# Kernel tuning notes

Measured on AMD Instinct MI355X. Metric: run time of the kernel, lower is better.

Reference implementation:

```python
import jax, jax.numpy as jnp
import numpy as np

B, C, W, H = 32, 128, 128, 128  # batch, channels, window_size, prediction_horizon
KAPPA = 10.0

def setup_inputs() -> dict:
    key = jax.random.key(0)
    k1, k2, k3, k4 = jax.random.split(key, 4)
    x_t = jax.random.normal(k1, (B, C, W), dtype=jnp.float32)
    # d are observation timestamps in [0, H), compared against ref_t = linspace(0, H, H)
    d = jax.random.uniform(k2, (B, C, W), dtype=jnp.float32) * H
    # m is an observation mask/weight in (0, 1]; avoid exact zeros for log(m)
    m = jax.random.uniform(k3, (B, C, W), dtype=jnp.float32, minval=1e-3, maxval=1.0)
    kernel = jax.random.normal(k4, (W,), dtype=jnp.float32) * 0.1
    return {"x_t": x_t, "d": d, "m": m, "kernel": kernel}

def reference(x_t, d, m, kernel):
    # ref_t: [H], matches torch.linspace(0, H, H)
    ref_t = jnp.linspace(0.0, H, H, dtype=x_t.dtype)
    # norm: [B,C,W,H] squared time differences
    norm = (d[..., None] - ref_t) ** 2
    alpha = jnp.log1p(jnp.exp(kernel))[None, None, :, None]  # softplus, [1,1,W,1]
    logm = jnp.log(m)[..., None]                             # [B,C,W,1]
    # low-intensity interpolation (softmax over window dim W)
    s = -alpha * norm + logm                                 # [B,C,W,H]
    w = jax.nn.logsumexp(s, axis=2)                          # [B,C,H]
    w1 = jnp.exp(s - w[:, :, None, :])                       # softmax weights
    y = jnp.einsum('bcwh,bcw->bch', w1, x_t)
    # high-intensity (transient) interpolation with sharper kernel kappa*alpha
    s_t = -KAPPA * alpha * norm + logm
    wt_lse = jax.nn.logsumexp(s_t, axis=2)
    w_t = jnp.exp(s_t - wt_lse[:, :, None, :])
    y_trans = jnp.einsum('bcwh,bcw->bch', w_t, x_t)
    return (y, w, y_trans)
```

## Files before the change

kernel.cpp:

```cpp
#include <hip/hip_runtime.h>
#include <hip/hip_bf16.h>

#define NB 32
#define NC 128
#define NW 128
#define NH 128
#define BCH (NB * NC * NH)

__global__ __launch_bounds__(128, 4) void sci_kernel(
    const void* __restrict__ xp, const void* __restrict__ dp,
    const void* __restrict__ mp, const void* __restrict__ kp,
    void* __restrict__ outp)
{
    const int bc   = blockIdx.x;
    const int tid  = threadIdx.x;
    const int lane = tid & 63;
    const int wid  = tid >> 6;

    __shared__ float4 tileS[NW];
    __shared__ float2 tileA[NW];
    __shared__ int    cum[NW + 1];
    __shared__ int    wtot[2];
    __shared__ float  wmin[2];

    const unsigned short* du16 = (const unsigned short*)dp;
    bool is_bf16 = true;
    #pragma unroll
    for (int i = 0; i < 32; i += 2) {
        float v = __uint_as_float(((unsigned int)du16[i]) << 16);
        is_bf16 = is_bf16 && (v >= 0.0f) && (v <= 129.0f);
    }

    float dv, mv, xv, kv;
    {
        const int base = bc * NW + tid;
        if (is_bf16) {
            dv = __bfloat162float(((const __hip_bfloat16*)dp)[base]);
            mv = __bfloat162float(((const __hip_bfloat16*)mp)[base]);
            xv = __bfloat162float(((const __hip_bfloat16*)xp)[base]);
            kv = __bfloat162float(((const __hip_bfloat16*)kp)[tid]);
        } else {
            dv = ((const float*)dp)[base];
            mv = ((const float*)mp)[base];
            xv = ((const float*)xp)[base];
            kv = ((const float*)kp)[tid];
        }
    }
    const float LOG2E = 1.4426950408889634f;
    float A2  = log1pf(__expf(kv)) * LOG2E;
    float sA2 = sqrtf(A2);
    float sd  = sA2 * dv;

    float rmn = sA2;
    #pragma unroll
    for (int o = 32; o >= 1; o >>= 1) rmn = fminf(rmn, __shfl_xor(rmn, o));
    if (lane == 0) wmin[wid] = rmn;

    cum[tid] = 0;
    __syncthreads();
    int bin  = min(127, max(0, (int)dv));
    int slot = atomicAdd(&cum[bin], 1);
    __syncthreads();

    int cnt = cum[tid];
    int c = cnt;
    #pragma unroll
    for (int o = 1; o < 64; o <<= 1) {
        int n = __shfl_up(c, o);
        if (lane >= o) c += n;
    }
    if (lane == 63) wtot[wid] = c;
    __syncthreads();
    int excl = c - cnt + (wid ? wtot[0] : 0);
    cum[tid] = excl;
    if (tid == 0) cum[NW] = NW;
    __syncthreads();

    int pos = cum[bin] + slot;
    tileS[pos] = make_float4(sA2, sd, mv, mv * xv);
    tileA[pos] = make_float2(sA2, sd);
    __syncthreads();

    const float rsA2min = (1.0f / fminf(wmin[0], wmin[1])) * 1.0005f;

    const float rh = (float)tid * (128.0f / 127.0f);

    int b0 = min(127, (int)rh);
    int s0, e0;
    {
        int r = 0;
        do {
            int lo = max(0, b0 - r);
            int hi = min(127, b0 + r);
            s0 = cum[lo]; e0 = cum[hi + 1];
            ++r;
        } while (s0 == e0);
    }
    float mn0 = 1e30f;
    for (int k = s0; k < e0; ++k) {
        float2 q = tileA[k];
        float t = __builtin_fmaf(-q.x, rh, q.y);
        mn0 = fminf(mn0, t * t);
    }

    float Rh = sqrtf(mn0 + 30.0f) * rsA2min;
    int lo = max(0, (int)(rh - Rh));
    int hi = min(127, (int)(rh + Rh));
    int ks = cum[lo], ke = cum[hi + 1];

    float mn = 1e30f;
    for (int k = ks; k < ke; ++k) {
        float2 q = tileA[k];
        float t = __builtin_fmaf(-q.x, rh, q.y);
        mn = fminf(mn, t * t);
    }

    float s1 = 0.f, a1 = 0.f, s2 = 0.f, a2 = 0.f;
    for (int k = ks; k < ke; ++k) {
        float4 q = tileS[k];
        float t  = __builtin_fmaf(-q.x, rh, q.y);
        float v  = __builtin_fmaf(-t, t, mn);
        float g1 = __builtin_amdgcn_exp2f(v);
        float sq = g1 * g1;
        float p4 = sq * sq;
        float p8 = p4 * p4;
        float g2 = p8 * sq;
        s1 = __builtin_fmaf(q.z, g1, s1);
        a1 = __builtin_fmaf(q.w, g1, a1);
        s2 = __builtin_fmaf(q.z, g2, s2);
        a2 = __builtin_fmaf(q.w, g2, a2);
    }

    const float LN2 = 0.6931471805599453f;
    float y  = a1 * __builtin_amdgcn_rcpf(s1);
    float wo = (__builtin_amdgcn_logf(s1) - mn) * LN2;
    float yt = a2 * __builtin_amdgcn_rcpf(s2);

    const int o = bc * NH + tid;
    if (is_bf16) {
        __hip_bfloat16* o16 = (__hip_bfloat16*)outp;
        o16[o]           = __float2bfloat16(y);
        o16[BCH + o]     = __float2bfloat16(wo);
        o16[2 * BCH + o] = __float2bfloat16(yt);
    } else {
        float* o32 = (float*)outp;
        o32[o]           = y;
        o32[BCH + o]     = wo;
        o32[2 * BCH + o] = yt;
    }
}

extern "C" void kernel_launch(void* const* d_in, const int* in_sizes, int n_in,
                              void* d_out, int out_size, void* d_ws, size_t ws_size,
                              hipStream_t stream) {
    const void* x_t = d_in[0];
    const void* d   = d_in[1];
    const void* m   = d_in[2];
    const void* k   = d_in[3];
    dim3 grid(NB * NC);
    dim3 block(128);
    hipLaunchKernelGGL(sci_kernel, grid, block, 0, stream, x_t, d, m, k, d_out);
}
```

Measured before the change: 76.16 us.

## Fuse min pass into online-softmax accumulation with 2x unrolled loop

Drops the separate pass that finds the minimum squared distance and folds it into the accumulation loop as an online rescaling, seeded with the coarse first-pass minimum. Removes the float2 shadow tile and reads the float4 tile instead, starts the nonempty-bin search at radius 2, and unrolls the main loop by two. The aim is fewer LDS passes and less shared memory. The cost is a data-dependent branch and extra rescale exps inside the hot loop.

```diff
diff --git a/kernel.cpp b/kernel.cpp
--- a/kernel.cpp
+++ b/kernel.cpp
@@ -18,7 +18,6 @@
     const int wid  = tid >> 6;
 
     __shared__ float4 tileS[NW];
-    __shared__ float2 tileA[NW];
     __shared__ int    cum[NW + 1];
     __shared__ int    wtot[2];
     __shared__ float  wmin[2];
@@ -78,7 +77,6 @@
 
     int pos = cum[bin] + slot;
     tileS[pos] = make_float4(sA2, sd, mv, mv * xv);
-    tileA[pos] = make_float2(sA2, sd);
     __syncthreads();
 
     const float rsA2min = (1.0f / fminf(wmin[0], wmin[1])) * 1.0005f;
@@ -88,17 +86,18 @@
     int b0 = min(127, (int)rh);
     int s0, e0;
     {
-        int r = 0;
-        do {
+        int r = 2;
+        for (;;) {
             int lo = max(0, b0 - r);
             int hi = min(127, b0 + r);
             s0 = cum[lo]; e0 = cum[hi + 1];
+            if (s0 != e0) break;
             ++r;
-        } while (s0 == e0);
+        }
     }
     float mn0 = 1e30f;
     for (int k = s0; k < e0; ++k) {
-        float2 q = tileA[k];
+        float4 q = tileS[k];
         float t = __builtin_fmaf(-q.x, rh, q.y);
         mn0 = fminf(mn0, t * t);
     }
@@ -108,27 +107,49 @@
     int hi = min(127, (int)(rh + Rh));
     int ks = cum[lo], ke = cum[hi + 1];
 
-    float mn = 1e30f;
-    for (int k = ks; k < ke; ++k) {
-        float2 q = tileA[k];
-        float t = __builtin_fmaf(-q.x, rh, q.y);
-        mn = fminf(mn, t * t);
-    }
-
+    float mn = mn0;
     float s1 = 0.f, a1 = 0.f, s2 = 0.f, a2 = 0.f;
-    for (int k = ks; k < ke; ++k) {
-        float4 q = tileS[k];
-        float t  = __builtin_fmaf(-q.x, rh, q.y);
-        float v  = __builtin_fmaf(-t, t, mn);
-        float g1 = __builtin_amdgcn_exp2f(v);
-        float sq = g1 * g1;
-        float p4 = sq * sq;
-        float p8 = p4 * p4;
-        float g2 = p8 * sq;
-        s1 = __builtin_fmaf(q.z, g1, s1);
-        a1 = __builtin_fmaf(q.w, g1, a1);
-        s2 = __builtin_fmaf(q.z, g2, s2);
-        a2 = __builtin_fmaf(q.w, g2, a2);
+    for (int k = ks; k < ke; k += 2) {
+        float4 qa = tileS[k];
+        int k1 = min(k + 1, NW - 1);
+        float4 qb = tileS[k1];
+        bool vb = (k + 1 < ke);
+        {
+            float t  = __builtin_fmaf(-qa.x, rh, qa.y);
+            float t2 = t * t;
+            if (t2 < mn) {
+                float f  = __builtin_amdgcn_exp2f(t2 - mn);
+                float fs = f * f, f4 = fs * fs, f8 = f4 * f4;
+                float f10 = f8 * fs;
+                s1 *= f; a1 *= f; s2 *= f10; a2 *= f10;
+                mn = t2;
+            }
+            float g1 = __builtin_amdgcn_exp2f(mn - t2);
+            float sq = g1 * g1, p4 = sq * sq, p8 = p4 * p4;
+            float g2 = p8 * sq;
+            s1 = __builtin_fmaf(qa.z, g1, s1);
+            a1 = __builtin_fmaf(qa.w, g1, a1);
+            s2 = __builtin_fmaf(qa.z, g2, s2);
+            a2 = __builtin_fmaf(qa.w, g2, a2);
+        }
+        if (vb) {
+            float t  = __builtin_fmaf(-qb.x, rh, qb.y);
+            float t2 = t * t;
+            if (t2 < mn) {
+                float f  = __builtin_amdgcn_exp2f(t2 - mn);
+                float fs = f * f, f4 = fs * fs, f8 = f4 * f4;
+                float f10 = f8 * fs;
+                s1 *= f; a1 *= f; s2 *= f10; a2 *= f10;
+                mn = t2;
+            }
+            float g1 = __builtin_amdgcn_exp2f(mn - t2);
+            float sq = g1 * g1, p4 = sq * sq, p8 = p4 * p4;
+            float g2 = p8 * sq;
+            s1 = __builtin_fmaf(qb.z, g1, s1);
+            a1 = __builtin_fmaf(qb.w, g1, a1);
+            s2 = __builtin_fmaf(qb.z, g2, s2);
+            a2 = __builtin_fmaf(qb.w, g2, a2);
+        }
     }
 
     const float LN2 = 0.6931471805599453f;
```

New measurement: 73.30 us. -3.8%, faster.

## Fuse min pass into online-rescaled accumulation loop and drop duplicate shared tile

Applied to the files above, without the earlier changes.

Removes the separate pass that computed the exact minimum squared distance and instead keeps a running minimum, rescaling the accumulators whenever a smaller value appears (online-softmax style), with two elements processed per iteration into split accumulators. The float2 duplicate shared-memory tile is removed and all reads come from the float4 tile. The initial bin search also starts at radius 2. This cuts one LDS pass and a loop, in exchange for data-dependent rescale branches and more registers per thread.

```diff
diff --git a/kernel.cpp b/kernel.cpp
--- a/kernel.cpp
+++ b/kernel.cpp
@@ -18,7 +18,6 @@
     const int wid  = tid >> 6;
 
     __shared__ float4 tileS[NW];
-    __shared__ float2 tileA[NW];
     __shared__ int    cum[NW + 1];
     __shared__ int    wtot[2];
     __shared__ float  wmin[2];
@@ -78,7 +77,6 @@
 
     int pos = cum[bin] + slot;
     tileS[pos] = make_float4(sA2, sd, mv, mv * xv);
-    tileA[pos] = make_float2(sA2, sd);
     __syncthreads();
 
     const float rsA2min = (1.0f / fminf(wmin[0], wmin[1])) * 1.0005f;
@@ -88,17 +86,18 @@
     int b0 = min(127, (int)rh);
     int s0, e0;
     {
-        int r = 0;
-        do {
+        int r = 2;
+        for (;;) {
             int lo = max(0, b0 - r);
             int hi = min(127, b0 + r);
             s0 = cum[lo]; e0 = cum[hi + 1];
+            if (s0 != e0) break;
             ++r;
-        } while (s0 == e0);
+        }
     }
     float mn0 = 1e30f;
     for (int k = s0; k < e0; ++k) {
-        float2 q = tileA[k];
+        float4 q = tileS[k];
         float t = __builtin_fmaf(-q.x, rh, q.y);
         mn0 = fminf(mn0, t * t);
     }
@@ -108,28 +107,38 @@
     int hi = min(127, (int)(rh + Rh));
     int ks = cum[lo], ke = cum[hi + 1];
 
-    float mn = 1e30f;
-    for (int k = ks; k < ke; ++k) {
-        float2 q = tileA[k];
-        float t = __builtin_fmaf(-q.x, rh, q.y);
-        mn = fminf(mn, t * t);
+    float mn = mn0;
+    float s1x = 0.f, s1y = 0.f, a1x = 0.f, a1y = 0.f;
+    float s2x = 0.f, s2y = 0.f, a2x = 0.f, a2y = 0.f;
+    for (int k = ks; k < ke; k += 2) {
+        float4 qa = tileS[k];
+        float4 qb = tileS[min(k + 1, NW - 1)];
+        float tx = __builtin_fmaf(-qa.x, rh, qa.y);
+        float ty = __builtin_fmaf(-qb.x, rh, qb.y);
+        float t2x = tx * tx;
+        float t2y = (k + 1 < ke) ? ty * ty : 1e30f;
+        float pmin = fminf(t2x, t2y);
+        if (pmin < mn) {
+            float f  = __builtin_amdgcn_exp2f(pmin - mn);
+            float fs = f * f, f4 = fs * fs, f8 = f4 * f4;
+            float f10 = f8 * fs;
+            s1x *= f;   s1y *= f;   a1x *= f;   a1y *= f;
+            s2x *= f10; s2y *= f10; a2x *= f10; a2y *= f10;
+            mn = pmin;
+        }
+        float g1x = __builtin_amdgcn_exp2f(mn - t2x);
+        float g1y = __builtin_amdgcn_exp2f(mn - t2y);
+        float sqx = g1x * g1x, sqy = g1y * g1y;
+        float p4x = sqx * sqx, p4y = sqy * sqy;
+        float p8x = p4x * p4x, p8y = p4y * p4y;
+        float g2x = p8x * sqx, g2y = p8y * sqy;
+        s1x = __builtin_fmaf(qa.z, g1x, s1x);  s1y = __builtin_fmaf(qb.z, g1y, s1y);
+        a1x = __builtin_fmaf(qa.w, g1x, a1x);  a1y = __builtin_fmaf(qb.w, g1y, a1y);
+        s2x = __builtin_fmaf(qa.z, g2x, s2x);  s2y = __builtin_fmaf(qb.z, g2y, s2y);
+        a2x = __builtin_fmaf(qa.w, g2x, a2x);  a2y = __builtin_fmaf(qb.w, g2y, a2y);
     }
-
-    float s1 = 0.f, a1 = 0.f, s2 = 0.f, a2 = 0.f;
-    for (int k = ks; k < ke; ++k) {
-        float4 q = tileS[k];
-        float t  = __builtin_fmaf(-q.x, rh, q.y);
-        float v  = __builtin_fmaf(-t, t, mn);
-        float g1 = __builtin_amdgcn_exp2f(v);
-        float sq = g1 * g1;
-        float p4 = sq * sq;
-        float p8 = p4 * p4;
-        float g2 = p8 * sq;
-        s1 = __builtin_fmaf(q.z, g1, s1);
-        a1 = __builtin_fmaf(q.w, g1, a1);
-        s2 = __builtin_fmaf(q.z, g2, s2);
-        a2 = __builtin_fmaf(q.w, g2, a2);
-    }
+    float s1 = s1x + s1y, a1 = a1x + a1y;
+    float s2 = s2x + s2y, a2 = a2x + a2y;
 
     const float LN2 = 0.6931471805599453f;
     float y  = a1 * __builtin_amdgcn_rcpf(s1);
```

After: 73.29 us. 1.04x faster.

## Fuse min-search and accumulation with online rescaling over windowed bins

Applied to the files above, without the earlier changes.

Replaces the separate min-search passes over a float2 tile with a single online-softmax style accumulation that rescales running sums whenever a smaller squared distance appears. A seed window of at least ±2 bins is processed first, then the remaining range to a tighter cutoff (+12 instead of +30) is accumulated without revisiting the seed. The tileA shared array is removed and softplus is computed with hardware exp2/log intrinsics. The changes reduce LDS traffic and loop passes, but add divergent rescale branches and rely on the tighter cutoff still being accurate enough.

```diff
diff --git a/kernel.cpp b/kernel.cpp
--- a/kernel.cpp
+++ b/kernel.cpp
@@ -18,7 +18,6 @@
     const int wid  = tid >> 6;
 
     __shared__ float4 tileS[NW];
-    __shared__ float2 tileA[NW];
     __shared__ int    cum[NW + 1];
     __shared__ int    wtot[2];
     __shared__ float  wmin[2];
@@ -47,7 +46,8 @@
         }
     }
     const float LOG2E = 1.4426950408889634f;
-    float A2  = log1pf(__expf(kv)) * LOG2E;
+    float ex  = __builtin_amdgcn_exp2f(kv * LOG2E);
+    float A2  = __builtin_amdgcn_logf(1.0f + ex);
     float sA2 = sqrtf(A2);
     float sd  = sA2 * dv;
 
@@ -78,58 +78,54 @@
 
     int pos = cum[bin] + slot;
     tileS[pos] = make_float4(sA2, sd, mv, mv * xv);
-    tileA[pos] = make_float2(sA2, sd);
     __syncthreads();
 
     const float rsA2min = (1.0f / fminf(wmin[0], wmin[1])) * 1.0005f;
 
     const float rh = (float)tid * (128.0f / 127.0f);
 
-    int b0 = min(127, (int)rh);
-    int s0, e0;
-    {
-        int r = 0;
-        do {
-            int lo = max(0, b0 - r);
-            int hi = min(127, b0 + r);
-            s0 = cum[lo]; e0 = cum[hi + 1];
-            ++r;
-        } while (s0 == e0);
-    }
-    float mn0 = 1e30f;
-    for (int k = s0; k < e0; ++k) {
-        float2 q = tileA[k];
-        float t = __builtin_fmaf(-q.x, rh, q.y);
-        mn0 = fminf(mn0, t * t);
-    }
+    float mn = 1e30f;
+    float s1 = 0.f, a1 = 0.f, s2 = 0.f, a2 = 0.f;
 
-    float Rh = sqrtf(mn0 + 30.0f) * rsA2min;
-    int lo = max(0, (int)(rh - Rh));
-    int hi = min(127, (int)(rh + Rh));
-    int ks = cum[lo], ke = cum[hi + 1];
-
-    float mn = 1e30f;
-    for (int k = ks; k < ke; ++k) {
-        float2 q = tileA[k];
-        float t = __builtin_fmaf(-q.x, rh, q.y);
-        mn = fminf(mn, t * t);
-    }
-
-    float s1 = 0.f, a1 = 0.f, s2 = 0.f, a2 = 0.f;
-    for (int k = ks; k < ke; ++k) {
+    auto body = [&](int k) {
         float4 q = tileS[k];
         float t  = __builtin_fmaf(-q.x, rh, q.y);
-        float v  = __builtin_fmaf(-t, t, mn);
-        float g1 = __builtin_amdgcn_exp2f(v);
-        float sq = g1 * g1;
-        float p4 = sq * sq;
-        float p8 = p4 * p4;
+        float t2 = t * t;
+        if (t2 < mn) {
+            float f  = __builtin_amdgcn_exp2f(t2 - mn);
+            float fs = f * f, f4 = fs * fs, f8 = f4 * f4;
+            float f10 = f8 * fs;
+            s1 *= f; a1 *= f; s2 *= f10; a2 *= f10;
+            mn = t2;
+        }
+        float g1 = __builtin_amdgcn_exp2f(mn - t2);
+        float sq = g1 * g1, p4 = sq * sq, p8 = p4 * p4;
         float g2 = p8 * sq;
         s1 = __builtin_fmaf(q.z, g1, s1);
         a1 = __builtin_fmaf(q.w, g1, a1);
         s2 = __builtin_fmaf(q.z, g2, s2);
         a2 = __builtin_fmaf(q.w, g2, a2);
+    };
+
+    int b0 = min(127, (int)rh);
+    int lo0, hi0, s0, e0;
+    {
+        int r = 2;
+        for (;;) {
+            lo0 = max(0, b0 - r); hi0 = min(127, b0 + r);
+            s0 = cum[lo0]; e0 = cum[hi0 + 1];
+            if (s0 != e0) break;
+            ++r;
+        }
     }
+    for (int k = s0; k < e0; ++k) body(k);
+
+    float Rh = sqrtf(mn + 12.0f) * rsA2min;
+    int lo = min(lo0, max(0, (int)(rh - Rh)));
+    int hi = max(hi0, min(127, (int)(rh + Rh)));
+    int ks = cum[lo], ke = cum[hi + 1];
+    for (int k = ks; k < s0; ++k) body(k);
+    for (int k = e0; k < ke; ++k) body(k);
 
     const float LN2 = 0.6931471805599453f;
     float y  = a1 * __builtin_amdgcn_rcpf(s1);
```

Measured after the change: 72.88 us (median of 2 runs). 1.05x faster.
